# Optimization experiments

Measured on AMD Instinct MI355X. Metric: run time of the kernel, lower is better.

## Reference

```python
import jax, jax.numpy as jnp
import numpy as np

N_NODES = 100000
N_EDGES = 1600000
MSG = 16
HID = 16
N_ETYPE = 8
N_CLASSES = 40


def setup_inputs() -> dict:
    key = jax.random.key(0)
    ks = jax.random.split(key, 11)
    return {
        "features": jax.random.normal(ks[0], (N_NODES, HID), dtype=jnp.float32),
        "src": jax.random.randint(ks[1], (N_EDGES,), 0, N_NODES),
        "dst": jax.random.randint(ks[2], (N_EDGES,), 0, N_NODES),
        "etype": jax.random.randint(ks[3], (N_EDGES,), 0, N_ETYPE),
        "edge_matrix": jax.random.normal(ks[4], (N_ETYPE, MSG * HID), dtype=jnp.float32) * 0.1,
        "w_ih": jax.random.normal(ks[5], (3 * HID, MSG), dtype=jnp.float32) * 0.1,
        "w_hh": jax.random.normal(ks[6], (3 * HID, HID), dtype=jnp.float32) * 0.1,
        "b_ih": jax.random.normal(ks[7], (3 * HID,), dtype=jnp.float32) * 0.1,
        "b_hh": jax.random.normal(ks[8], (3 * HID,), dtype=jnp.float32) * 0.1,
        "out_w": jax.random.normal(ks[9], (N_CLASSES, HID), dtype=jnp.float32) * 0.1,
        "out_b": jax.random.normal(ks[10], (N_CLASSES,), dtype=jnp.float32) * 0.1,
    }


def reference(features, src, dst, etype, edge_matrix, w_ih, w_hh, b_ih, b_hh, out_w, out_b):
    n = features.shape[0]
    # message: per-edge [MSG,HID] matrix (gathered by edge type) times src h
    A = edge_matrix[etype].reshape(-1, MSG, HID)          # [E, MSG, HID]
    msg = jnp.einsum('emh,eh->em', A, features[src])      # [E, MSG]
    # reduce: scatter-sum messages onto destination nodes
    m = jax.ops.segment_sum(msg, dst, num_segments=n)     # [N, MSG]
    # apply: one GRU step per node (PyTorch nn.GRU gate math)
    gi = m @ w_ih.T + b_ih                                # [N, 3*HID]
    gh = features @ w_hh.T + b_hh                         # [N, 3*HID]
    i_r, i_z, i_n = jnp.split(gi, 3, axis=-1)
    h_r, h_z, h_n = jnp.split(gh, 3, axis=-1)
    r = jax.nn.sigmoid(i_r + h_r)
    z = jax.nn.sigmoid(i_z + h_z)
    c = jnp.tanh(i_n + r * h_n)
    h = (1.0 - z) * c + z * features                      # [N, HID]
    return h @ out_w.T + out_b                            # [N, N_CLASSES]
```

## Files before the change

kernel.cpp:

```cpp
#include <hip/hip_runtime.h>
#include <math.h>

constexpr int N_NODES   = 100000;
constexpr int N_EDGES   = 1600000;
constexpr int MSG       = 16;
constexpr int HID       = 16;
constexpr int N_ETYPE   = 8;
constexpr int N_CLASSES = 40;

constexpr int CBSIZE   = 256;
constexpr int NBUCKET  = (N_NODES + CBSIZE - 1) / CBSIZE;
constexpr int SBSIZE   = 32;
constexpr int NSUB     = 8;
constexpr int NSB      = NBUCKET * NSUB;
constexpr int EPB      = 4096;
constexpr int NEBLK    = (N_EDGES + EPB - 1) / EPB;
constexpr int REC_CAP  = 5120;
constexpr int FGRID    = 1024;
constexpr int NSLOT    = 2048;
constexpr int A_STRIDE = 260;

__device__ __forceinline__ float sigmoidf_(float x) { return 1.0f / (1.0f + __expf(-x)); }
__device__ __forceinline__ float tanhf_(float x) { float e = __expf(2.0f * x); return 1.0f - 2.0f / (e + 1.0f); }

__device__ __forceinline__ unsigned f2bf(float f) {
    unsigned u = __float_as_uint(f);
    return (u + 0x7FFFu + ((u >> 16) & 1u)) >> 16;
}
__device__ __forceinline__ float bflo(unsigned u) { return __uint_as_float(u << 16); }
__device__ __forceinline__ float bfhi(unsigned u) { return __uint_as_float(u & 0xFFFF0000u); }

__global__ void __launch_bounds__(256) cvt_kernel(const float* __restrict__ features,
                                                  uint4* __restrict__ featb,
                                                  int* __restrict__ gcursor) {
    int i = blockIdx.x * 256 + threadIdx.x;
    if (i < NBUCKET) gcursor[i] = i * REC_CAP;
    if (i * 8 >= N_NODES * HID) return;
    const float4* fp = reinterpret_cast<const float4*>(features + i * 8);
    float4 a = fp[0], b = fp[1];
    uint4 o;
    o.x = f2bf(a.x) | (f2bf(a.y) << 16);
    o.y = f2bf(a.z) | (f2bf(a.w) << 16);
    o.z = f2bf(b.x) | (f2bf(b.y) << 16);
    o.w = f2bf(b.z) | (f2bf(b.w) << 16);
    featb[i] = o;
}

__global__ void __launch_bounds__(512) partition_kernel(
    const int* __restrict__ src,
    const int* __restrict__ dst,
    const int* __restrict__ etype,
    int* __restrict__ gcursor,
    int* __restrict__ records)
{
    __shared__ int srec[EPB];
    __shared__ unsigned short sbkt[EPB];
    __shared__ int lh[NBUCKET];
    __shared__ int lscan[NBUCKET];
    __shared__ int lofs[NBUCKET];
    __shared__ int gbarr[NBUCKET];
    __shared__ int sscan[512];

    int t = threadIdx.x;
    int base = blockIdx.x * EPB;

    for (int i = t; i < NBUCKET; i += 512) lh[i] = 0;
    __syncthreads();

    int rr[8]; int bb[8];
    #pragma unroll
    for (int q = 0; q < 8; ++q) {
        int e = base + t + 512 * q;
        if (e < N_EDGES) {
            int d = dst[e];
            bb[q] = d >> 8;
            rr[q] = (src[e] << 11) | (etype[e] << 8) | (d & 255);
            atomicAdd(&lh[bb[q]], 1);
        } else bb[q] = -1;
    }
    __syncthreads();

    int i0 = t * 4;
    int v0 = 0, v1 = 0, v2 = 0, v3 = 0;
    if (i0     < NBUCKET) v0 = lh[i0];
    if (i0 + 1 < NBUCKET) v1 = lh[i0 + 1];
    if (i0 + 2 < NBUCKET) v2 = lh[i0 + 2];
    if (i0 + 3 < NBUCKET) v3 = lh[i0 + 3];
    int tsum = v0 + v1 + v2 + v3;
    sscan[t] = tsum;
    __syncthreads();
    for (int off = 1; off < 512; off <<= 1) {
        int tmp = (t >= off) ? sscan[t - off] : 0;
        __syncthreads();
        sscan[t] += tmp;
        __syncthreads();
    }
    int excl = sscan[t] - tsum;
    if (i0     < NBUCKET) { lscan[i0]     = excl; lofs[i0]     = excl; gbarr[i0]     = v0 ? atomicAdd(&gcursor[i0],     v0) : 0; } excl += v0;
    if (i0 + 1 < NBUCKET) { lscan[i0 + 1] = excl; lofs[i0 + 1] = excl; gbarr[i0 + 1] = v1 ? atomicAdd(&gcursor[i0 + 1], v1) : 0; } excl += v1;
    if (i0 + 2 < NBUCKET) { lscan[i0 + 2] = excl; lofs[i0 + 2] = excl; gbarr[i0 + 2] = v2 ? atomicAdd(&gcursor[i0 + 2], v2) : 0; } excl += v2;
    if (i0 + 3 < NBUCKET) { lscan[i0 + 3] = excl; lofs[i0 + 3] = excl; gbarr[i0 + 3] = v3 ? atomicAdd(&gcursor[i0 + 3], v3) : 0; }
    __syncthreads();

    #pragma unroll
    for (int q = 0; q < 8; ++q) {
        if (bb[q] >= 0) {
            int sidx = atomicAdd(&lofs[bb[q]], 1);
            srec[sidx] = rr[q];
            sbkt[sidx] = (unsigned short)bb[q];
        }
    }
    __syncthreads();

    int cnt = min(EPB, N_EDGES - base);
    for (int s2 = t; s2 < cnt; s2 += 512) {
        int b2 = sbkt[s2];
        int pos = gbarr[b2] + (s2 - lscan[b2]);
        if (pos < (b2 + 1) * REC_CAP)
            records[pos] = srec[s2];
    }
}

__global__ void __launch_bounds__(256) partition2_kernel(
    const int* __restrict__ gcursor,
    const int* __restrict__ records,
    int* __restrict__ records2,
    int* __restrict__ slot_off)
{
    __shared__ int hist[NSLOT];
    __shared__ int sscan[256];
    __shared__ int srec[REC_CAP];

    int cb = blockIdx.x;
    int beg = cb * REC_CAP;
    int cnt = min(gcursor[cb] - beg, REC_CAP);
    int t = threadIdx.x;

    #pragma unroll
    for (int j = 0; j < 8; ++j) hist[t * 8 + j] = 0;
    __syncthreads();

    for (int i = t; i < cnt; i += 256) {
        int r = records[beg + i];
        atomicAdd(&hist[((r & 255) << 3) | ((r >> 8) & 7)], 1);
    }
    __syncthreads();

    int loc[8]; int tsum = 0;
    #pragma unroll
    for (int j = 0; j < 8; ++j) { loc[j] = hist[t * 8 + j]; tsum += loc[j]; }
    sscan[t] = tsum;
    __syncthreads();
    for (int off = 1; off < 256; off <<= 1) {
        int tmp = (t >= off) ? sscan[t - off] : 0;
        __syncthreads();
        sscan[t] += tmp;
        __syncthreads();
    }
    int excl = sscan[t] - tsum;
    #pragma unroll
    for (int j = 0; j < 8; ++j) {
        slot_off[cb * (NSLOT + 1) + t * 8 + j] = beg + excl;
        hist[t * 8 + j] = excl;
        excl += loc[j];
    }
    if (t == 0) slot_off[cb * (NSLOT + 1) + NSLOT] = beg + cnt;
    __syncthreads();

    for (int i = t; i < cnt; i += 256) {
        int r = records[beg + i];
        int pos = atomicAdd(&hist[((r & 255) << 3) | ((r >> 8) & 7)], 1);
        srec[pos] = r;
    }
    __syncthreads();
    for (int i = t; i < cnt; i += 256) records2[beg + i] = srec[i];
}

__global__ void __launch_bounds__(256, 4) fused_kernel(
    const uint4* __restrict__ featb,
    const float* __restrict__ features,
    const int*   __restrict__ slot_off,
    const int*   __restrict__ records2,
    const float* __restrict__ edge_matrix,
    const float* __restrict__ w_ih,
    const float* __restrict__ w_hh,
    const float* __restrict__ b_ih,
    const float* __restrict__ b_hh,
    const float* __restrict__ out_w,
    const float* __restrict__ out_b,
    float*       __restrict__ out)
{
    __shared__ float A[N_ETYPE * A_STRIDE];
    __shared__ float hnT[HID][SBSIZE + 1];
    __shared__ float outS[SBSIZE * 44];
    __shared__ float wihL[3 * HID * 17];
    __shared__ float whhL[3 * HID * 17];
    __shared__ float outwL[N_CLASSES * 17];
    __shared__ float bihL[3 * HID];
    __shared__ float bhhL[3 * HID];
    __shared__ float outbL[N_CLASSES];

    int t = threadIdx.x;
    int dl = t >> 3, q = t & 7;
    const float4* feat4 = reinterpret_cast<const float4*>(features);

    for (int i = t; i < N_ETYPE * MSG * HID; i += 256)
        A[(i >> 8) * A_STRIDE + (i & 255)] = edge_matrix[i];
    for (int i = t; i < 3 * HID * MSG; i += 256) wihL[(i >> 4) * 17 + (i & 15)] = w_ih[i];
    for (int i = t; i < 3 * HID * HID; i += 256) whhL[(i >> 4) * 17 + (i & 15)] = w_hh[i];
    for (int i = t; i < N_CLASSES * HID; i += 256) outwL[(i >> 4) * 17 + (i & 15)] = out_w[i];
    if (t < 48) bihL[t] = b_ih[t];
    else if (t < 96) bhhL[t - 48] = b_hh[t - 48];
    else if (t < 136) outbL[t - 96] = out_b[t - 96];

    for (int b = blockIdx.x; b < NSB; b += FGRID) {
        int nodeBase = b * SBSIZE;
        if (nodeBase >= N_NODES) continue;
        int cb = b >> 3, sb = b & 7;
        __syncthreads();

        int go = cb * (NSLOT + 1) + sb * 256 + t;
        int begin = slot_off[go], end = slot_off[go + 1];

        float acc[16];
        #pragma unroll
        for (int k = 0; k < 16; ++k) acc[k] = 0.0f;
        for (int i = begin; i < end; ++i) {
            int rec = records2[i];
            int sn = rec >> 11;
            uint4 ua = featb[2 * sn], ub = featb[2 * sn + 1];
            acc[0]  += bflo(ua.x); acc[1]  += bfhi(ua.x);
            acc[2]  += bflo(ua.y); acc[3]  += bfhi(ua.y);
            acc[4]  += bflo(ua.z); acc[5]  += bfhi(ua.z);
            acc[6]  += bflo(ua.w); acc[7]  += bfhi(ua.w);
            acc[8]  += bflo(ub.x); acc[9]  += bfhi(ub.x);
            acc[10] += bflo(ub.y); acc[11] += bfhi(ub.y);
            acc[12] += bflo(ub.z); acc[13] += bfhi(ub.z);
            acc[14] += bflo(ub.w); acc[15] += bfhi(ub.w);
        }

        float p[16];
        {
            const float* Aq = &A[q * A_STRIDE];
            #pragma unroll
            for (int mm = 0; mm < 16; ++mm) {
                const float4* Ar = reinterpret_cast<const float4*>(Aq + mm * 16);
                float4 x0 = Ar[0], x1 = Ar[1], x2 = Ar[2], x3 = Ar[3];
                p[mm] = x0.x*acc[0]  + x0.y*acc[1]  + x0.z*acc[2]  + x0.w*acc[3]
                      + x1.x*acc[4]  + x1.y*acc[5]  + x1.z*acc[6]  + x1.w*acc[7]
                      + x2.x*acc[8]  + x2.y*acc[9]  + x2.z*acc[10] + x2.w*acc[11]
                      + x3.x*acc[12] + x3.y*acc[13] + x3.z*acc[14] + x3.w*acc[15];
            }
        }
        #pragma unroll
        for (int mm = 0; mm < 16; ++mm) {
            p[mm] += __shfl_xor(p[mm], 1, 64);
            p[mm] += __shfl_xor(p[mm], 2, 64);
            p[mm] += __shfl_xor(p[mm], 4, 64);
        }

        int n = nodeBase + dl;
        float hva[16];
        {
            const float4* hp = feat4 + (size_t)n * 4;
            float4 h0 = hp[0], h1 = hp[1], h2 = hp[2], h3 = hp[3];
            hva[0]=h0.x; hva[1]=h0.y; hva[2]=h0.z; hva[3]=h0.w;
            hva[4]=h1.x; hva[5]=h1.y; hva[6]=h1.z; hva[7]=h1.w;
            hva[8]=h2.x; hva[9]=h2.y; hva[10]=h2.z; hva[11]=h2.w;
            hva[12]=h3.x; hva[13]=h3.y; hva[14]=h3.z; hva[15]=h3.w;
        }
        #pragma unroll
        for (int jj = 0; jj < 2; ++jj) {
            int j = 2 * q + jj;
            float ir  = bihL[j];
            float iz  = bihL[j + HID];
            float inn = bihL[j + 2 * HID];
            float hr  = bhhL[j];
            float hz  = bhhL[j + HID];
            float hnn = bhhL[j + 2 * HID];
            const float* wir = &wihL[j * 17];
            const float* wiz = &wihL[(j + HID) * 17];
            const float* win = &wihL[(j + 2 * HID) * 17];
            const float* whr = &whhL[j * 17];
            const float* whz = &whhL[(j + HID) * 17];
            const float* whn = &whhL[(j + 2 * HID) * 17];
            #pragma unroll
            for (int k = 0; k < HID; ++k) {
                ir  += wir[k] * p[k];
                iz  += wiz[k] * p[k];
                inn += win[k] * p[k];
                hr  += whr[k] * hva[k];
                hz  += whz[k] * hva[k];
                hnn += whn[k] * hva[k];
            }
            float rg = sigmoidf_(ir + hr);
            float zg = sigmoidf_(iz + hz);
            float cg = tanhf_(inn + rg * hnn);
            hnT[j][dl] = (1.0f - zg) * cg + zg * hva[j];
        }
        __syncthreads();

        {
            float hh[HID];
            #pragma unroll
            for (int k = 0; k < HID; ++k) hh[k] = hnT[k][dl];
            #pragma unroll
            for (int cc = 0; cc < 5; ++cc) {
                int c = 5 * q + cc;
                float a2 = outbL[c];
                const float* wr = &outwL[c * 17];
                #pragma unroll
                for (int k = 0; k < HID; ++k) a2 += wr[k] * hh[k];
                outS[dl * 44 + c] = a2;
            }
        }
        __syncthreads();

        {
            float4* ob4 = reinterpret_cast<float4*>(out + (size_t)nodeBase * N_CLASSES);
            #pragma unroll
            for (int rep = 0; rep < 2; ++rep) {
                int i = t + rep * 256;
                if (i < SBSIZE * N_CLASSES / 4) {
                    int node = i / 10, qq = i - node * 10;
                    ob4[i] = *reinterpret_cast<const float4*>(&outS[node * 44 + qq * 4]);
                }
            }
        }
    }
}

extern "C" void kernel_launch(void* const* d_in, const int* in_sizes, int n_in,
                              void* d_out, int out_size, void* d_ws, size_t ws_size,
                              hipStream_t stream) {
    const float* features    = (const float*)d_in[0];
    const int*   src         = (const int*)  d_in[1];
    const int*   dst         = (const int*)  d_in[2];
    const int*   etype       = (const int*)  d_in[3];
    const float* edge_matrix = (const float*)d_in[4];
    const float* w_ih        = (const float*)d_in[5];
    const float* w_hh        = (const float*)d_in[6];
    const float* b_ih        = (const float*)d_in[7];
    const float* b_hh        = (const float*)d_in[8];
    const float* out_w       = (const float*)d_in[9];
    const float* out_b       = (const float*)d_in[10];
    float* out = (float*)d_out;

    int* gcursor  = (int*)d_ws;
    int* slot_off = gcursor + NBUCKET;
    int* records  = slot_off + NBUCKET * (NSLOT + 1);
    int* records2 = records + NBUCKET * REC_CAP;
    size_t featb_off = ((size_t)((char*)(records2 + NBUCKET * REC_CAP) - (char*)d_ws) + 15) & ~15ull;
    uint4* featb = (uint4*)((char*)d_ws + featb_off);

    cvt_kernel<<<(N_NODES * HID / 8 + 255) / 256, 256, 0, stream>>>(features, featb, gcursor);
    partition_kernel<<<NEBLK, 512, 0, stream>>>(src, dst, etype, gcursor, records);
    partition2_kernel<<<NBUCKET, 256, 0, stream>>>(gcursor, records, records2, slot_off);
    fused_kernel<<<FGRID, 256, 0, stream>>>(
        featb, features, slot_off, records2, edge_matrix,
        w_ih, w_hh, b_ih, b_hh, out_w, out_b, out);
}
```

Before: 110.8 us.

## Use wave-shuffle scans, stage edge records in LDS, and drop GRU-output LDS round-trips

Both partition kernels replace their multi-barrier shared-memory Hillis-Steele scan with a wave-level shuffle scan plus a small per-wave sum array. The first partition kernel also reuses the rank returned by the histogram atomics instead of doing a second atomic pass. The fused kernel cooperatively loads each sub-block's edge records into LDS with nontemporal loads. It broadcasts the new hidden state across lanes with shuffles instead of a transposed LDS buffer, writes outputs directly with nontemporal scalar stores instead of staged float4 stores, and raises the grid size and occupancy hint. These cut barriers and LDS traffic, but the scattered 4-byte output stores may coalesce worse than the previous float4 writes.

```diff
diff --git a/kernel.cpp b/kernel.cpp
--- a/kernel.cpp
+++ b/kernel.cpp
@@ -16,9 +16,10 @@
 constexpr int EPB      = 4096;
 constexpr int NEBLK    = (N_EDGES + EPB - 1) / EPB;
 constexpr int REC_CAP  = 5120;
-constexpr int FGRID    = 1024;
+constexpr int FGRID    = 1536;
 constexpr int NSLOT    = 2048;
 constexpr int A_STRIDE = 260;
+constexpr int SRECC    = 1792;
 
 __device__ __forceinline__ float sigmoidf_(float x) { return 1.0f / (1.0f + __expf(-x)); }
 __device__ __forceinline__ float tanhf_(float x) { float e = __expf(2.0f * x); return 1.0f - 2.0f / (e + 1.0f); }
@@ -57,9 +58,8 @@
     __shared__ unsigned short sbkt[EPB];
     __shared__ int lh[NBUCKET];
     __shared__ int lscan[NBUCKET];
-    __shared__ int lofs[NBUCKET];
     __shared__ int gbarr[NBUCKET];
-    __shared__ int sscan[512];
+    __shared__ int wsum[8];
 
     int t = threadIdx.x;
     int base = blockIdx.x * EPB;
@@ -67,7 +67,7 @@
     for (int i = t; i < NBUCKET; i += 512) lh[i] = 0;
     __syncthreads();
 
-    int rr[8]; int bb[8];
+    int rr[8]; int bb[8]; int rk[8];
     #pragma unroll
     for (int q = 0; q < 8; ++q) {
         int e = base + t + 512 * q;
@@ -75,7 +75,7 @@
             int d = dst[e];
             bb[q] = d >> 8;
             rr[q] = (src[e] << 11) | (etype[e] << 8) | (d & 255);
-            atomicAdd(&lh[bb[q]], 1);
+            rk[q] = atomicAdd(&lh[bb[q]], 1);
         } else bb[q] = -1;
     }
     __syncthreads();
@@ -87,25 +87,31 @@
     if (i0 + 2 < NBUCKET) v2 = lh[i0 + 2];
     if (i0 + 3 < NBUCKET) v3 = lh[i0 + 3];
     int tsum = v0 + v1 + v2 + v3;
-    sscan[t] = tsum;
-    __syncthreads();
-    for (int off = 1; off < 512; off <<= 1) {
-        int tmp = (t >= off) ? sscan[t - off] : 0;
-        __syncthreads();
-        sscan[t] += tmp;
-        __syncthreads();
-    }
-    int excl = sscan[t] - tsum;
-    if (i0     < NBUCKET) { lscan[i0]     = excl; lofs[i0]     = excl; gbarr[i0]     = v0 ? atomicAdd(&gcursor[i0],     v0) : 0; } excl += v0;
-    if (i0 + 1 < NBUCKET) { lscan[i0 + 1] = excl; lofs[i0 + 1] = excl; gbarr[i0 + 1] = v1 ? atomicAdd(&gcursor[i0 + 1], v1) : 0; } excl += v1;
-    if (i0 + 2 < NBUCKET) { lscan[i0 + 2] = excl; lofs[i0 + 2] = excl; gbarr[i0 + 2] = v2 ? atomicAdd(&gcursor[i0 + 2], v2) : 0; } excl += v2;
-    if (i0 + 3 < NBUCKET) { lscan[i0 + 3] = excl; lofs[i0 + 3] = excl; gbarr[i0 + 3] = v3 ? atomicAdd(&gcursor[i0 + 3], v3) : 0; }
+
+    int lane = t & 63, w = t >> 6;
+    int inc = tsum;
+    #pragma unroll
+    for (int off = 1; off < 64; off <<= 1) {
+        int u = __shfl_up(inc, off, 64);
+        if (lane >= off) inc += u;
+    }
+    if (lane == 63) wsum[w] = inc;
+    __syncthreads();
+    int basew = 0;
+    #pragma unroll
+    for (int i = 0; i < 8; ++i) if (i < w) basew += wsum[i];
+    int excl = basew + inc - tsum;
+
+    if (i0     < NBUCKET) { lscan[i0]     = excl; gbarr[i0]     = v0 ? atomicAdd(&gcursor[i0],     v0) : 0; } excl += v0;
+    if (i0 + 1 < NBUCKET) { lscan[i0 + 1] = excl; gbarr[i0 + 1] = v1 ? atomicAdd(&gcursor[i0 + 1], v1) : 0; } excl += v1;
+    if (i0 + 2 < NBUCKET) { lscan[i0 + 2] = excl; gbarr[i0 + 2] = v2 ? atomicAdd(&gcursor[i0 + 2], v2) : 0; } excl += v2;
+    if (i0 + 3 < NBUCKET) { lscan[i0 + 3] = excl; gbarr[i0 + 3] = v3 ? atomicAdd(&gcursor[i0 + 3], v3) : 0; }
     __syncthreads();
 
     #pragma unroll
     for (int q = 0; q < 8; ++q) {
         if (bb[q] >= 0) {
-            int sidx = atomicAdd(&lofs[bb[q]], 1);
+            int sidx = lscan[bb[q]] + rk[q];
             srec[sidx] = rr[q];
             sbkt[sidx] = (unsigned short)bb[q];
         }
@@ -128,7 +134,7 @@
     int* __restrict__ slot_off)
 {
     __shared__ int hist[NSLOT];
-    __shared__ int sscan[256];
+    __shared__ int wsum[4];
     __shared__ int srec[REC_CAP];
 
     int cb = blockIdx.x;
@@ -149,15 +155,21 @@
     int loc[8]; int tsum = 0;
     #pragma unroll
     for (int j = 0; j < 8; ++j) { loc[j] = hist[t * 8 + j]; tsum += loc[j]; }
-    sscan[t] = tsum;
-    __syncthreads();
-    for (int off = 1; off < 256; off <<= 1) {
-        int tmp = (t >= off) ? sscan[t - off] : 0;
-        __syncthreads();
-        sscan[t] += tmp;
-        __syncthreads();
-    }
-    int excl = sscan[t] - tsum;
+
+    int lane = t & 63, w = t >> 6;
+    int inc = tsum;
+    #pragma unroll
+    for (int off = 1; off < 64; off <<= 1) {
+        int u = __shfl_up(inc, off, 64);
+        if (lane >= off) inc += u;
+    }
+    if (lane == 63) wsum[w] = inc;
+    __syncthreads();
+    int basew = 0;
+    #pragma unroll
+    for (int i = 0; i < 4; ++i) if (i < w) basew += wsum[i];
+    int excl = basew + inc - tsum;
+
     #pragma unroll
     for (int j = 0; j < 8; ++j) {
         slot_off[cb * (NSLOT + 1) + t * 8 + j] = beg + excl;
@@ -176,7 +188,7 @@
     for (int i = t; i < cnt; i += 256) records2[beg + i] = srec[i];
 }
 
-__global__ void __launch_bounds__(256, 4) fused_kernel(
+__global__ void __launch_bounds__(256, 6) fused_kernel(
     const uint4* __restrict__ featb,
     const float* __restrict__ features,
     const int*   __restrict__ slot_off,
@@ -191,14 +203,13 @@
     float*       __restrict__ out)
 {
     __shared__ float A[N_ETYPE * A_STRIDE];
-    __shared__ float hnT[HID][SBSIZE + 1];
-    __shared__ float outS[SBSIZE * 44];
     __shared__ float wihL[3 * HID * 17];
     __shared__ float whhL[3 * HID * 17];
     __shared__ float outwL[N_CLASSES * 17];
     __shared__ float bihL[3 * HID];
     __shared__ float bhhL[3 * HID];
     __shared__ float outbL[N_CLASSES];
+    __shared__ int   srecL[SRECC];
 
     int t = threadIdx.x;
     int dl = t >> 3, q = t & 7;
@@ -219,14 +230,22 @@
         int cb = b >> 3, sb = b & 7;
         __syncthreads();
 
-        int go = cb * (NSLOT + 1) + sb * 256 + t;
-        int begin = slot_off[go], end = slot_off[go + 1];
+        int sobase = cb * (NSLOT + 1) + sb * 256;
+        int S0 = slot_off[sobase];
+        int S1 = slot_off[sobase + 256];
+        int begin = slot_off[sobase + t];
+        int end   = slot_off[sobase + t + 1];
+        int lim = min(S1 - S0, SRECC);
+        for (int i = t; i < lim; i += 256)
+            srecL[i] = __builtin_nontemporal_load(records2 + S0 + i);
+        __syncthreads();
 
         float acc[16];
         #pragma unroll
         for (int k = 0; k < 16; ++k) acc[k] = 0.0f;
         for (int i = begin; i < end; ++i) {
-            int rec = records2[i];
+            int li = i - S0;
+            int rec = (li < SRECC) ? srecL[li] : records2[i];
             int sn = rec >> 11;
             uint4 ua = featb[2 * sn], ub = featb[2 * sn + 1];
             acc[0]  += bflo(ua.x); acc[1]  += bfhi(ua.x);
@@ -269,6 +288,7 @@
             hva[8]=h2.x; hva[9]=h2.y; hva[10]=h2.z; hva[11]=h2.w;
             hva[12]=h3.x; hva[13]=h3.y; hva[14]=h3.z; hva[15]=h3.w;
         }
+        float hg[2];
         #pragma unroll
         for (int jj = 0; jj < 2; ++jj) {
             int j = 2 * q + jj;
@@ -296,36 +316,27 @@
             float rg = sigmoidf_(ir + hr);
             float zg = sigmoidf_(iz + hz);
             float cg = tanhf_(inn + rg * hnn);
-            hnT[j][dl] = (1.0f - zg) * cg + zg * hva[j];
-        }
-        __syncthreads();
-
-        {
-            float hh[HID];
+            float hj = features[(size_t)n * HID + j];
+            hg[jj] = (1.0f - zg) * cg + zg * hj;
+        }
+
+        int lanebase = (t & 63) & 56;
+        float hh[16];
+        #pragma unroll
+        for (int qq = 0; qq < 8; ++qq) {
+            hh[2 * qq]     = __shfl(hg[0], lanebase + qq, 64);
+            hh[2 * qq + 1] = __shfl(hg[1], lanebase + qq, 64);
+        }
+
+        float* op = out + (size_t)n * N_CLASSES + 5 * q;
+        #pragma unroll
+        for (int cc = 0; cc < 5; ++cc) {
+            int c = 5 * q + cc;
+            float a2 = outbL[c];
+            const float* wr = &outwL[c * 17];
             #pragma unroll
-            for (int k = 0; k < HID; ++k) hh[k] = hnT[k][dl];
-            #pragma unroll
-            for (int cc = 0; cc < 5; ++cc) {
-                int c = 5 * q + cc;
-                float a2 = outbL[c];
-                const float* wr = &outwL[c * 17];
-                #pragma unroll
-                for (int k = 0; k < HID; ++k) a2 += wr[k] * hh[k];
-                outS[dl * 44 + c] = a2;
-            }
-        }
-        __syncthreads();
-
-        {
-            float4* ob4 = reinterpret_cast<float4*>(out + (size_t)nodeBase * N_CLASSES);
-            #pragma unroll
-            for (int rep = 0; rep < 2; ++rep) {
-                int i = t + rep * 256;
-                if (i < SBSIZE * N_CLASSES / 4) {
-                    int node = i / 10, qq = i - node * 10;
-                    ob4[i] = *reinterpret_cast<const float4*>(&outS[node * 44 + qq * 4]);
-                }
-            }
+            for (int k = 0; k < HID; ++k) a2 += wr[k] * hh[k];
+            __builtin_nontemporal_store(a2, op + cc);
         }
     }
 }
```

Measured after the change: 119.6 us. 8.0% more time.
